# Performance work log

Hardware: AMD Instinct MI355X
Metric: run time of the kernel (lower is better)

The kernel has to match this reference:

```python
import jax, jax.numpy as jnp
import numpy as np

N_NODES = 8      # objects per graph (fixed in source)
N_AT = 16        # anchors/targets vocab: 8 colors + 8 markers
H = 128          # n_hidden
BS = 16384


def _mlp(x, W1, b1, W2, b2):
    # layers.fully_connected default activation is relu; second layer linear.
    # dropout is identity in eval mode.
    return jax.nn.relu(x @ W1 + b1) @ W2 + b2


def _edges_and_segments(bs):
    # static edge list: all ordered pairs (i,j), i != j, per graph, offset per batch
    ii, jj = np.meshgrid(np.arange(N_NODES), np.arange(N_NODES), indexing='ij')
    m = ii != jj
    base = np.stack([ii[m], jj[m]], axis=1)                      # [56, 2]
    offs = (np.arange(bs) * N_NODES)[:, None, None]
    edges = (base[None] + offs).reshape(-1, 2).astype(np.int32)  # [bs*56, 2]
    seg_ids = np.repeat(np.arange(bs), N_NODES).astype(np.int32) # [bs*8]
    return jnp.asarray(edges), jnp.asarray(seg_ids)


def setup_inputs() -> dict:
    key = jax.random.key(0)
    ks = jax.random.split(key, 14)

    anchors = jax.random.randint(ks[0], (BS,), 0, N_AT)
    n_jumps = jax.random.randint(ks[1], (BS,), 0, N_NODES)
    positions = jax.random.uniform(ks[2], (BS, N_NODES, 2), dtype=jnp.float32)
    colors = jax.random.randint(ks[3], (BS, N_NODES), 0, 8)
    markers = jax.random.randint(ks[4], (BS, N_NODES), 8, 16)  # markers live in [8,16)

    def lin(k, fan_in, fan_out):
        return jax.random.normal(k, (fan_in, fan_out), dtype=jnp.float32) / np.sqrt(fan_in)

    d_in = 2 + 8 + 8 + N_AT + N_NODES  # pos + color_oh + marker_oh + question(16+8) = 42
    z = lambda n: jnp.zeros((n,), jnp.float32)
    return {
        'anchors': anchors, 'n_jumps': n_jumps, 'positions': positions,
        'colors': colors, 'markers': markers,
        'pre_W1': lin(ks[5], d_in, H),     'pre_b1': z(H),
        'pre_W2': lin(ks[6], H, H),        'pre_b2': z(H),
        'msg_W1': lin(ks[7], 2 * H + 1, H),'msg_b1': z(H),
        'msg_W2': lin(ks[8], H, H),        'msg_b2': z(H),
        'post_W1': lin(ks[9], 2 * H, H),   'post_b1': z(H),
        'post_W2': lin(ks[10], H, H),      'post_b2': z(H),
        'out_W1': lin(ks[11], H, H),       'out_b1': z(H),
        'out_W2': lin(ks[12], H, N_AT),    'out_b2': z(N_AT),
    }


def reference(anchors, n_jumps, positions, colors, markers,
              pre_W1, pre_b1, pre_W2, pre_b2,
              msg_W1, msg_b1, msg_W2, msg_b2,
              post_W1, post_b1, post_W2, post_b2,
              out_W1, out_b1, out_W2, out_b2):
    bs = positions.shape[0]
    edges, seg_ids = _edges_and_segments(bs)
    n_total = bs * N_NODES

    col_oh = jax.nn.one_hot(colors, 8, dtype=jnp.float32).reshape(n_total, 8)
    mrk_oh = jax.nn.one_hot(markers - 8, 8, dtype=jnp.float32).reshape(n_total, 8)
    pos = positions.reshape(n_total, 2)

    # pairwise euclidean distance per edge -> [E, 1]
    dp = pos[edges[:, 0]] - pos[edges[:, 1]]
    dist = jnp.sqrt(jnp.sum(dp * dp, axis=1, keepdims=True))

    # question broadcast to every node of its graph
    q = jnp.concatenate([jax.nn.one_hot(anchors, N_AT, dtype=jnp.float32),
                         jax.nn.one_hot(n_jumps, N_NODES, dtype=jnp.float32)], axis=1)
    q = q[seg_ids]  # [bs*8, 24]

    x0 = _mlp(jnp.concatenate([pos, col_oh, mrk_oh, q], axis=1),
              pre_W1, pre_b1, pre_W2, pre_b2)  # [bs*8, H]

    # one message-passing step: gather -> MLP -> scatter(segment_sum on source idx)
    mi = jnp.concatenate([x0[edges[:, 0]], x0[edges[:, 1]], dist], axis=1)  # [E, 257]
    msgs = _mlp(mi, msg_W1, msg_b1, msg_W2, msg_b2)                          # [E, H]
    upd = jax.ops.segment_sum(msgs, edges[:, 0], num_segments=n_total)       # [bs*8, H]

    x = _mlp(jnp.concatenate([upd, x0], axis=1), post_W1, post_b1, post_W2, post_b2)

    logits = jax.ops.segment_sum(x, seg_ids, num_segments=bs)  # [bs, H]
    logits = _mlp(logits, out_W1, out_b1, out_W2, out_b2)      # [bs, 16]
    return logits
```

## Files before the change

kernel.cpp:

```cpp
#include <hip/hip_runtime.h>

#define LROW 136

typedef __bf16 bf16x8 __attribute__((ext_vector_type(8)));
typedef float  f32x4  __attribute__((ext_vector_type(4)));

#define MFMA16(a, b, c) __builtin_amdgcn_mfma_f32_16x16x32_bf16((a), (b), (c), 0, 0, 0)

__device__ __forceinline__ unsigned short f2bf(float f) {
  unsigned u = __float_as_uint(f);
  u += 0x7fffu + ((u >> 16) & 1u);
  return (unsigned short)(u >> 16);
}
__device__ __forceinline__ float bflo(unsigned v) { return __uint_as_float(v << 16); }
__device__ __forceinline__ float bfhi(unsigned v) { return __uint_as_float(v & 0xffff0000u); }

__global__ void combine_weights(
    const float* __restrict__ pre_W2, const float* __restrict__ msg_W1,
    const float* __restrict__ msg_W2, const float* __restrict__ post_W1,
    const float* __restrict__ post_W2, const float* __restrict__ out_W1,
    const float* __restrict__ out_W2, const float* __restrict__ pre_b2,
    const float* __restrict__ msg_b1, const float* __restrict__ msg_b2,
    const float* __restrict__ post_b1, const float* __restrict__ post_b2,
    const float* __restrict__ out_b1,
    unsigned short* __restrict__ WabT, unsigned short* __restrict__ WdT,
    unsigned short* __restrict__ WcT, unsigned short* __restrict__ WoT,
    unsigned short* __restrict__ Wo2T, float* __restrict__ vecs)
{
  __shared__ float part[256];
  const int b = blockIdx.x;
  const int t = threadIdx.x;
  if (b < 320) {
    const int p  = b >> 6;
    const int kp = b & 63;
    const int k  = kp * 2 + (t >> 7);
    const int n  = t & 127;
    const float* L; const float* R; unsigned short* O;
    if (p == 0)      { L = pre_W2;  R = msg_W1;             O = WabT; }
    else if (p == 1) { L = pre_W2;  R = msg_W1 + 128*128;   O = WabT + 128*128; }
    else if (p == 2) { L = pre_W2;  R = post_W1 + 128*128;  O = WdT; }
    else if (p == 3) { L = msg_W2;  R = post_W1;            O = WcT; }
    else             { L = post_W2; R = out_W1;             O = WoT; }
    const float* Lr = L + k * 128;
    float a0 = 0.f, a1 = 0.f, a2 = 0.f, a3 = 0.f;
    #pragma unroll 8
    for (int m = 0; m < 128; m += 4) {
      a0 = fmaf(Lr[m + 0], R[(m + 0) * 128 + n], a0);
      a1 = fmaf(Lr[m + 1], R[(m + 1) * 128 + n], a1);
      a2 = fmaf(Lr[m + 2], R[(m + 2) * 128 + n], a2);
      a3 = fmaf(Lr[m + 3], R[(m + 3) * 128 + n], a3);
    }
    O[n * 128 + k] = f2bf((a0 + a1) + (a2 + a3));
  } else if (b == 320) {
    for (int idx = t; idx < 16 * 128; idx += 256) {
      int o = idx >> 7, k = idx & 127;
      Wo2T[o * 128 + k] = f2bf(out_W2[k * 16 + o]);
    }
    if (t < 128) vecs[t] = msg_W1[256 * 128 + t];
  } else {
    const int n = t & 127;
    const int h = t >> 7;
    float s = 0.f;
    if (b == 321) {
      #pragma unroll 8
      for (int m = h * 64; m < h * 64 + 64; ++m)
        s = fmaf(pre_b2[m], msg_W1[m * 128 + n] + msg_W1[(128 + m) * 128 + n], s);
    } else if (b == 322) {
      #pragma unroll 8
      for (int m = h * 64; m < h * 64 + 64; ++m) {
        s = fmaf(7.f * msg_b2[m], post_W1[m * 128 + n], s);
        s = fmaf(pre_b2[m], post_W1[(128 + m) * 128 + n], s);
      }
    } else {
      #pragma unroll 8
      for (int m = h * 64; m < h * 64 + 64; ++m)
        s = fmaf(8.f * post_b2[m], out_W1[m * 128 + n], s);
    }
    part[t] = s;
    __syncthreads();
    if (t < 128) {
      float r = part[t] + part[t + 128];
      if (b == 321)      vecs[128 + t] = r + msg_b1[t];
      else if (b == 322) vecs[256 + t] = r + post_b1[t];
      else               vecs[384 + t] = r + out_b1[t];
    }
  }
}

__global__ void __launch_bounds__(256, 3) rrn_main(
    const int* __restrict__ anchors, const int* __restrict__ n_jumps,
    const float* __restrict__ positions, const int* __restrict__ colors,
    const int* __restrict__ markers, const float* __restrict__ pre_W1,
    const float* __restrict__ pre_b1,
    const unsigned short* __restrict__ WabT, const unsigned short* __restrict__ WdT,
    const unsigned short* __restrict__ WcT, const unsigned short* __restrict__ WoT,
    const unsigned short* __restrict__ Wo2T, const float* __restrict__ vecs,
    const float* __restrict__ out_b2, float* __restrict__ out)
{
  __shared__ __align__(16) char smem[54272];
  unsigned short* Ab  = (unsigned short*)(smem);
  unsigned short* Bb  = (unsigned short*)(smem + 17408);
  float* sW1          = (float*)(smem);
  float* posL         = (float*)(smem + 22016);
  int*   cmk          = (int*)(smem + 22528);
  int*   ganj         = (int*)(smem + 22784);
  unsigned short* h1  = (unsigned short*)(smem + 34816);
  unsigned short* Sph = (unsigned short*)(smem + 34816);
  unsigned short* hob = (unsigned short*)(smem + 39168);
  float* dist         = (float*)(smem + 52224);

  const int tid  = threadIdx.x;
  const int lane = tid & 63;
  const int w    = tid >> 6;
  const int l15  = lane & 15;
  const int quad = lane >> 4;
  const int g0   = blockIdx.x * 8;
  const int n0   = blockIdx.x * 64;

  for (int i = tid; i < 43 * 128; i += 256)
    sW1[i] = (i < 42 * 128) ? pre_W1[i] : pre_b1[i - 42 * 128];
  if (tid < 128) posL[tid] = positions[n0 * 2 + tid];
  else if (tid < 192) {
    int node = tid - 128;
    cmk[node] = colors[n0 + node] | ((markers[n0 + node] - 8) << 8);
  } else if (tid < 200) {
    int g = tid - 192;
    ganj[g] = anchors[g0 + g] | (n_jumps[g0 + g] << 8);
  }
  for (int i = tid; i < 512; i += 256) {
    int g = i >> 6, ii = (i >> 3) & 7, jj = i & 7;
    const float* pa = positions + (n0 + g * 8 + ii) * 2;
    const float* pb = positions + (n0 + g * 8 + jj) * 2;
    float dx = pa[0] - pb[0], dy = pa[1] - pb[1];
    dist[i] = sqrtf(dx * dx + dy * dy);
  }
  __syncthreads();

  {
    const int n  = tid & 127;
    const int rh = tid >> 7;
    for (int rr = 0; rr < 32; ++rr) {
      int r = rh * 32 + rr;
      float px = posL[r * 2], py = posL[r * 2 + 1];
      int cm = cmk[r], gn = ganj[r >> 3];
      int c = cm & 255, mk = cm >> 8;
      int a = gn & 255, nj = gn >> 8;
      float acc = sW1[42 * 128 + n]
                + px * sW1[n] + py * sW1[128 + n]
                + sW1[(2 + c) * 128 + n] + sW1[(10 + mk) * 128 + n]
                + sW1[(18 + a) * 128 + n] + sW1[(34 + nj) * 128 + n];
      h1[r * LROW + n] = f2bf(fmaxf(acc, 0.f));
    }
  }
  __syncthreads();

  f32x4 accAB[4][4];
  f32x4 accD[4][2];
  {
    f32x4 zero = {0.f, 0.f, 0.f, 0.f};
    #pragma unroll
    for (int mt = 0; mt < 4; ++mt) {
      #pragma unroll
      for (int nt = 0; nt < 4; ++nt) accAB[mt][nt] = zero;
      accD[mt][0] = zero; accD[mt][1] = zero;
    }
  }
  #pragma unroll
  for (int kb = 0; kb < 128; kb += 32) {
    const int ko = kb + quad * 8;
    bf16x8 fa[4], fb[4], fd[2];
    #pragma unroll
    for (int mt = 0; mt < 4; ++mt)
      fa[mt] = *(const bf16x8*)&h1[(mt * 16 + l15) * LROW + ko];
    #pragma unroll
    for (int nt = 0; nt < 4; ++nt)
      fb[nt] = *(const bf16x8*)&WabT[(w * 64 + nt * 16 + l15) * 128 + ko];
    #pragma unroll
    for (int dt = 0; dt < 2; ++dt)
      fd[dt] = *(const bf16x8*)&WdT[(w * 32 + dt * 16 + l15) * 128 + ko];
    #pragma unroll
    for (int mt = 0; mt < 4; ++mt) {
      #pragma unroll
      for (int nt = 0; nt < 4; ++nt)
        accAB[mt][nt] = MFMA16(fa[mt], fb[nt], accAB[mt][nt]);
      accD[mt][0] = MFMA16(fa[mt], fd[0], accD[mt][0]);
      accD[mt][1] = MFMA16(fa[mt], fd[1], accD[mt][1]);
    }
  }
  {
    unsigned short* dstbuf = (w < 2) ? Ab : Bb;
    const int cb = (w & 1) * 64;
    #pragma unroll
    for (int mt = 0; mt < 4; ++mt)
      #pragma unroll
      for (int nt = 0; nt < 4; ++nt) {
        int col = cb + nt * 16 + l15;
        #pragma unroll
        for (int r = 0; r < 4; ++r)
          dstbuf[(mt * 16 + quad * 4 + r) * LROW + col] = f2bf(accAB[mt][nt][r]);
      }
  }
  __syncthreads();

  {
    const int g   = tid >> 5;
    const int nb4 = (tid & 31) * 4;
    const float4 w1d4 = *(const float4*)&vecs[nb4];
    const float4 cab4 = *(const float4*)&vecs[128 + nb4];
    float B0[8], B1[8], B2[8], B3[8];
    #pragma unroll
    for (int j = 0; j < 8; ++j) {
      uint2 vb = *(const uint2*)&Bb[(g * 8 + j) * LROW + nb4];
      B0[j] = bflo(vb.x); B1[j] = bfhi(vb.x);
      B2[j] = bflo(vb.y); B3[j] = bfhi(vb.y);
    }
    #pragma unroll
    for (int i = 0; i < 8; ++i) {
      uint2 va = *(const uint2*)&Ab[(g * 8 + i) * LROW + nb4];
      float a0 = bflo(va.x) + cab4.x, a1 = bfhi(va.x) + cab4.y;
      float a2 = bflo(va.y) + cab4.z, a3 = bfhi(va.y) + cab4.w;
      float s0 = 0.f, s1 = 0.f, s2 = 0.f, s3 = 0.f;
      #pragma unroll
      for (int j = 0; j < 8; ++j) {
        if (j == i) continue;
        float d = dist[g * 64 + i * 8 + j];
        s0 += fmaxf(fmaf(d, w1d4.x, B0[j]) + a0, 0.f);
        s1 += fmaxf(fmaf(d, w1d4.y, B1[j]) + a1, 0.f);
        s2 += fmaxf(fmaf(d, w1d4.z, B2[j]) + a2, 0.f);
        s3 += fmaxf(fmaf(d, w1d4.w, B3[j]) + a3, 0.f);
      }
      uint2 o;
      o.x = (unsigned)f2bf(s0) | ((unsigned)f2bf(s1) << 16);
      o.y = (unsigned)f2bf(s2) | ((unsigned)f2bf(s3) << 16);
      *(uint2*)&Ab[(g * 8 + i) * LROW + nb4] = o;
    }
  }
  __syncthreads();

  {
    const unsigned short* Sb = Ab;
    #pragma unroll
    for (int kb = 0; kb < 128; kb += 32) {
      const int ko = kb + quad * 8;
      bf16x8 fa[4], fc[2];
      #pragma unroll
      for (int mt = 0; mt < 4; ++mt)
        fa[mt] = *(const bf16x8*)&Sb[(mt * 16 + l15) * LROW + ko];
      #pragma unroll
      for (int dt = 0; dt < 2; ++dt)
        fc[dt] = *(const bf16x8*)&WcT[(w * 32 + dt * 16 + l15) * 128 + ko];
      #pragma unroll
      for (int mt = 0; mt < 4; ++mt) {
        accD[mt][0] = MFMA16(fa[mt], fc[0], accD[mt][0]);
        accD[mt][1] = MFMA16(fa[mt], fc[1], accD[mt][1]);
      }
    }
    #pragma unroll
    for (int mt = 0; mt < 4; ++mt)
      #pragma unroll
      for (int dt = 0; dt < 2; ++dt) {
        int col = w * 32 + dt * 16 + l15;
        float cp = vecs[256 + col];
        f32x4 a = accD[mt][dt];
        float s = fmaxf(a[0] + cp, 0.f) + fmaxf(a[1] + cp, 0.f)
                + fmaxf(a[2] + cp, 0.f) + fmaxf(a[3] + cp, 0.f);
        s += __shfl_xor(s, 16);
        int grow = mt * 2 + (lane >= 32 ? 1 : 0);
        if ((lane & 31) < 16) Sph[grow * LROW + col] = f2bf(s);
        else                  Sph[(8 + grow) * LROW + col] = 0;
      }
  }
  __syncthreads();

  {
    f32x4 acco[2];
    f32x4 zero = {0.f, 0.f, 0.f, 0.f};
    acco[0] = zero; acco[1] = zero;
    #pragma unroll
    for (int kb = 0; kb < 128; kb += 32) {
      const int ko = kb + quad * 8;
      bf16x8 fa = *(const bf16x8*)&Sph[l15 * LROW + ko];
      #pragma unroll
      for (int dt = 0; dt < 2; ++dt) {
        bf16x8 fbv = *(const bf16x8*)&WoT[(w * 32 + dt * 16 + l15) * 128 + ko];
        acco[dt] = MFMA16(fa, fbv, acco[dt]);
      }
    }
    #pragma unroll
    for (int dt = 0; dt < 2; ++dt) {
      int col = w * 32 + dt * 16 + l15;
      float co = vecs[384 + col];
      #pragma unroll
      for (int r = 0; r < 4; ++r)
        hob[(quad * 4 + r) * LROW + col] = f2bf(fmaxf(acco[dt][r] + co, 0.f));
    }
  }
  __syncthreads();

  if (w == 0) {
    f32x4 accf = {0.f, 0.f, 0.f, 0.f};
    #pragma unroll
    for (int kb = 0; kb < 128; kb += 32) {
      const int ko = kb + quad * 8;
      bf16x8 fa  = *(const bf16x8*)&hob[l15 * LROW + ko];
      bf16x8 fbv = *(const bf16x8*)&Wo2T[l15 * 128 + ko];
      accf = MFMA16(fa, fbv, accf);
    }
    if (quad < 2) {
      float b2 = out_b2[l15];
      #pragma unroll
      for (int r = 0; r < 4; ++r) {
        int row = quad * 4 + r;
        out[(g0 + row) * 16 + l15] = accf[r] + b2;
      }
    }
  }
}

extern "C" void kernel_launch(void* const* d_in, const int* in_sizes, int n_in,
                              void* d_out, int out_size, void* d_ws, size_t ws_size,
                              hipStream_t stream) {
  const int*   anchors   = (const int*)d_in[0];
  const int*   n_jumps   = (const int*)d_in[1];
  const float* positions = (const float*)d_in[2];
  const int*   colors    = (const int*)d_in[3];
  const int*   markers   = (const int*)d_in[4];
  const float* pre_W1  = (const float*)d_in[5];
  const float* pre_b1  = (const float*)d_in[6];
  const float* pre_W2  = (const float*)d_in[7];
  const float* pre_b2  = (const float*)d_in[8];
  const float* msg_W1  = (const float*)d_in[9];
  const float* msg_b1  = (const float*)d_in[10];
  const float* msg_W2  = (const float*)d_in[11];
  const float* msg_b2  = (const float*)d_in[12];
  const float* post_W1 = (const float*)d_in[13];
  const float* post_b1 = (const float*)d_in[14];
  const float* post_W2 = (const float*)d_in[15];
  const float* post_b2 = (const float*)d_in[16];
  const float* out_W1  = (const float*)d_in[17];
  const float* out_b1  = (const float*)d_in[18];
  const float* out_W2  = (const float*)d_in[19];
  const float* out_b2  = (const float*)d_in[20];

  char* ws = (char*)d_ws;
  unsigned short* WabT = (unsigned short*)(ws);
  unsigned short* WdT  = (unsigned short*)(ws + 65536);
  unsigned short* WcT  = (unsigned short*)(ws + 98304);
  unsigned short* WoT  = (unsigned short*)(ws + 131072);
  unsigned short* Wo2T = (unsigned short*)(ws + 163840);
  float*          vecs = (float*)(ws + 167936);

  const int BS = in_sizes[0];

  combine_weights<<<324, 256, 0, stream>>>(
      pre_W2, msg_W1, msg_W2, post_W1, post_W2, out_W1, out_W2,
      pre_b2, msg_b1, msg_b2, post_b1, post_b2, out_b1,
      WabT, WdT, WcT, WoT, Wo2T, vecs);

  rrn_main<<<BS / 8, 256, 0, stream>>>(
      anchors, n_jumps, positions, colors, markers, pre_W1, pre_b1,
      WabT, WdT, WcT, WoT, Wo2T, vecs, out_b2, (float*)d_out);
}
```

Before: 177.7 us.

## Shrink shared memory and split first GEMM to fit four blocks per CU

Cuts LDS from about 54KB to 38KB by precomputing a per-graph question row (bias plus anchor and jump rows of pre_W1), so only 18 rows of pre_W1 are staged. Buffers are overlapped more aggressively and the vecs constants are cached in shared memory. The A/B and D projections are split into two MFMA passes with staged writeback and an extra barrier, which lowers live accumulator registers so launch bounds can rise to 4 blocks per CU. Float-to-bf16 conversion now uses the native __bf16 cast instead of manual rounding. The risk is more barriers and serialised MFMA phases.

```diff
diff --git a/kernel.cpp b/kernel.cpp
--- a/kernel.cpp
+++ b/kernel.cpp
@@ -2,18 +2,20 @@
 
 #define LROW 136
 
-typedef __bf16 bf16x8 __attribute__((ext_vector_type(8)));
-typedef float  f32x4  __attribute__((ext_vector_type(4)));
+typedef __bf16 bf16x8  __attribute__((ext_vector_type(8)));
+typedef __bf16 bf16x4v __attribute__((ext_vector_type(4)));
+typedef float  f32x4   __attribute__((ext_vector_type(4)));
 
 #define MFMA16(a, b, c) __builtin_amdgcn_mfma_f32_16x16x32_bf16((a), (b), (c), 0, 0, 0)
 
-__device__ __forceinline__ unsigned short f2bf(float f) {
+__device__ __forceinline__ float bflo(unsigned v) { return __uint_as_float(v << 16); }
+__device__ __forceinline__ float bfhi(unsigned v) { return __uint_as_float(v & 0xffff0000u); }
+
+__device__ __forceinline__ unsigned short f2bf_u16(float f) {
   unsigned u = __float_as_uint(f);
   u += 0x7fffu + ((u >> 16) & 1u);
   return (unsigned short)(u >> 16);
 }
-__device__ __forceinline__ float bflo(unsigned v) { return __uint_as_float(v << 16); }
-__device__ __forceinline__ float bfhi(unsigned v) { return __uint_as_float(v & 0xffff0000u); }
 
 __global__ void combine_weights(
     const float* __restrict__ pre_W2, const float* __restrict__ msg_W1,
@@ -50,11 +52,11 @@
       a2 = fmaf(Lr[m + 2], R[(m + 2) * 128 + n], a2);
       a3 = fmaf(Lr[m + 3], R[(m + 3) * 128 + n], a3);
     }
-    O[n * 128 + k] = f2bf((a0 + a1) + (a2 + a3));
+    O[n * 128 + k] = f2bf_u16((a0 + a1) + (a2 + a3));
   } else if (b == 320) {
     for (int idx = t; idx < 16 * 128; idx += 256) {
       int o = idx >> 7, k = idx & 127;
-      Wo2T[o * 128 + k] = f2bf(out_W2[k * 16 + o]);
+      Wo2T[o * 128 + k] = f2bf_u16(out_W2[k * 16 + o]);
     }
     if (t < 128) vecs[t] = msg_W1[256 * 128 + t];
   } else {
@@ -87,45 +89,51 @@
   }
 }
 
-__global__ void __launch_bounds__(256, 3) rrn_main(
+__global__ void __launch_bounds__(256, 4) rrn_main(
     const int* __restrict__ anchors, const int* __restrict__ n_jumps,
     const float* __restrict__ positions, const int* __restrict__ colors,
     const int* __restrict__ markers, const float* __restrict__ pre_W1,
     const float* __restrict__ pre_b1,
-    const unsigned short* __restrict__ WabT, const unsigned short* __restrict__ WdT,
-    const unsigned short* __restrict__ WcT, const unsigned short* __restrict__ WoT,
-    const unsigned short* __restrict__ Wo2T, const float* __restrict__ vecs,
+    const __bf16* __restrict__ WabT, const __bf16* __restrict__ WdT,
+    const __bf16* __restrict__ WcT, const __bf16* __restrict__ WoT,
+    const __bf16* __restrict__ Wo2T, const float* __restrict__ vecs,
     const float* __restrict__ out_b2, float* __restrict__ out)
 {
-  __shared__ __align__(16) char smem[54272];
-  unsigned short* Ab  = (unsigned short*)(smem);
-  unsigned short* Bb  = (unsigned short*)(smem + 17408);
-  float* sW1          = (float*)(smem);
-  float* posL         = (float*)(smem + 22016);
-  int*   cmk          = (int*)(smem + 22528);
-  int*   ganj         = (int*)(smem + 22784);
-  unsigned short* h1  = (unsigned short*)(smem + 34816);
-  unsigned short* Sph = (unsigned short*)(smem + 34816);
-  unsigned short* hob = (unsigned short*)(smem + 39168);
-  float* dist         = (float*)(smem + 52224);
+  __shared__ __align__(16) char smem[38912];
+  __bf16* Ab   = (__bf16*)(smem);
+  float*  sW1s = (float*)(smem);
+  float*  qrow = (float*)(smem + 9216);
+  float*  posL = (float*)(smem + 13312);
+  int*    cmk  = (int*)(smem + 13824);
+  __bf16* h1   = (__bf16*)(smem + 17408);
+  __bf16* Bb   = (__bf16*)(smem + 17408);
+  __bf16* Sph  = (__bf16*)(smem + 17408);
+  __bf16* hob  = (__bf16*)(smem + 21760);
+  float*  dist = (float*)(smem + 34816);
+  float*  vec  = (float*)(smem + 36864);
 
   const int tid  = threadIdx.x;
   const int lane = tid & 63;
   const int w    = tid >> 6;
   const int l15  = lane & 15;
   const int quad = lane >> 4;
+  const int colw = w * 32;
   const int g0   = blockIdx.x * 8;
   const int n0   = blockIdx.x * 64;
 
-  for (int i = tid; i < 43 * 128; i += 256)
-    sW1[i] = (i < 42 * 128) ? pre_W1[i] : pre_b1[i - 42 * 128];
+  for (int i = tid; i < 18 * 128; i += 256) sW1s[i] = pre_W1[i];
+  {
+    const int n = tid & 127;
+    for (int g = (tid >> 7); g < 8; g += 2) {
+      int a = anchors[g0 + g], nj = n_jumps[g0 + g];
+      qrow[g * 128 + n] = pre_b1[n] + pre_W1[(18 + a) * 128 + n]
+                        + pre_W1[(34 + nj) * 128 + n];
+    }
+  }
   if (tid < 128) posL[tid] = positions[n0 * 2 + tid];
   else if (tid < 192) {
     int node = tid - 128;
     cmk[node] = colors[n0 + node] | ((markers[n0 + node] - 8) << 8);
-  } else if (tid < 200) {
-    int g = tid - 192;
-    ganj[g] = anchors[g0 + g] | (n_jumps[g0 + g] << 8);
   }
   for (int i = tid; i < 512; i += 256) {
     int g = i >> 6, ii = (i >> 3) & 7, jj = i & 7;
@@ -134,6 +142,7 @@
     float dx = pa[0] - pb[0], dy = pa[1] - pb[1];
     dist[i] = sqrtf(dx * dx + dy * dy);
   }
+  for (int i = tid; i < 512; i += 256) vec[i] = vecs[i];
   __syncthreads();
 
   {
@@ -142,71 +151,89 @@
     for (int rr = 0; rr < 32; ++rr) {
       int r = rh * 32 + rr;
       float px = posL[r * 2], py = posL[r * 2 + 1];
-      int cm = cmk[r], gn = ganj[r >> 3];
+      int cm = cmk[r];
       int c = cm & 255, mk = cm >> 8;
-      int a = gn & 255, nj = gn >> 8;
-      float acc = sW1[42 * 128 + n]
-                + px * sW1[n] + py * sW1[128 + n]
-                + sW1[(2 + c) * 128 + n] + sW1[(10 + mk) * 128 + n]
-                + sW1[(18 + a) * 128 + n] + sW1[(34 + nj) * 128 + n];
-      h1[r * LROW + n] = f2bf(fmaxf(acc, 0.f));
-    }
-  }
-  __syncthreads();
-
-  f32x4 accAB[4][4];
-  f32x4 accD[4][2];
+      float acc = qrow[(r >> 3) * 128 + n]
+                + px * sW1s[n] + py * sW1s[128 + n]
+                + sW1s[(2 + c) * 128 + n] + sW1s[(10 + mk) * 128 + n];
+      h1[r * LROW + n] = (__bf16)fmaxf(acc, 0.f);
+    }
+  }
+  __syncthreads();
+
+  f32x4 acc1[4][4];
   {
     f32x4 zero = {0.f, 0.f, 0.f, 0.f};
     #pragma unroll
-    for (int mt = 0; mt < 4; ++mt) {
-      #pragma unroll
-      for (int nt = 0; nt < 4; ++nt) accAB[mt][nt] = zero;
-      accD[mt][0] = zero; accD[mt][1] = zero;
-    }
+    for (int mt = 0; mt < 4; ++mt)
+      #pragma unroll
+      for (int nt = 0; nt < 4; ++nt) acc1[mt][nt] = zero;
   }
   #pragma unroll
   for (int kb = 0; kb < 128; kb += 32) {
     const int ko = kb + quad * 8;
-    bf16x8 fa[4], fb[4], fd[2];
+    bf16x8 fa[4], fb[4];
     #pragma unroll
     for (int mt = 0; mt < 4; ++mt)
       fa[mt] = *(const bf16x8*)&h1[(mt * 16 + l15) * LROW + ko];
-    #pragma unroll
-    for (int nt = 0; nt < 4; ++nt)
-      fb[nt] = *(const bf16x8*)&WabT[(w * 64 + nt * 16 + l15) * 128 + ko];
-    #pragma unroll
-    for (int dt = 0; dt < 2; ++dt)
-      fd[dt] = *(const bf16x8*)&WdT[(w * 32 + dt * 16 + l15) * 128 + ko];
+    fb[0] = *(const bf16x8*)&WabT[(colw + l15) * 128 + ko];
+    fb[1] = *(const bf16x8*)&WabT[(colw + 16 + l15) * 128 + ko];
+    fb[2] = *(const bf16x8*)&WabT[(128 + colw + l15) * 128 + ko];
+    fb[3] = *(const bf16x8*)&WabT[(128 + colw + 16 + l15) * 128 + ko];
+    #pragma unroll
+    for (int mt = 0; mt < 4; ++mt)
+      #pragma unroll
+      for (int nt = 0; nt < 4; ++nt)
+        acc1[mt][nt] = MFMA16(fa[mt], fb[nt], acc1[mt][nt]);
+  }
+  #pragma unroll
+  for (int mt = 0; mt < 4; ++mt)
+    #pragma unroll
+    for (int nt = 0; nt < 2; ++nt) {
+      int col = colw + nt * 16 + l15;
+      #pragma unroll
+      for (int r = 0; r < 4; ++r)
+        Ab[(mt * 16 + quad * 4 + r) * LROW + col] = (__bf16)acc1[mt][nt][r];
+    }
+
+  f32x4 accD[4][2];
+  {
+    f32x4 zero = {0.f, 0.f, 0.f, 0.f};
+    #pragma unroll
+    for (int mt = 0; mt < 4; ++mt) { accD[mt][0] = zero; accD[mt][1] = zero; }
+  }
+  #pragma unroll
+  for (int kb = 0; kb < 128; kb += 32) {
+    const int ko = kb + quad * 8;
+    bf16x8 fa[4], fd[2];
+    #pragma unroll
+    for (int mt = 0; mt < 4; ++mt)
+      fa[mt] = *(const bf16x8*)&h1[(mt * 16 + l15) * LROW + ko];
+    fd[0] = *(const bf16x8*)&WdT[(colw + l15) * 128 + ko];
+    fd[1] = *(const bf16x8*)&WdT[(colw + 16 + l15) * 128 + ko];
     #pragma unroll
     for (int mt = 0; mt < 4; ++mt) {
-      #pragma unroll
-      for (int nt = 0; nt < 4; ++nt)
-        accAB[mt][nt] = MFMA16(fa[mt], fb[nt], accAB[mt][nt]);
       accD[mt][0] = MFMA16(fa[mt], fd[0], accD[mt][0]);
       accD[mt][1] = MFMA16(fa[mt], fd[1], accD[mt][1]);
     }
   }
-  {
-    unsigned short* dstbuf = (w < 2) ? Ab : Bb;
-    const int cb = (w & 1) * 64;
-    #pragma unroll
-    for (int mt = 0; mt < 4; ++mt)
-      #pragma unroll
-      for (int nt = 0; nt < 4; ++nt) {
-        int col = cb + nt * 16 + l15;
-        #pragma unroll
-        for (int r = 0; r < 4; ++r)
-          dstbuf[(mt * 16 + quad * 4 + r) * LROW + col] = f2bf(accAB[mt][nt][r]);
-      }
-  }
+  __syncthreads();
+  #pragma unroll
+  for (int mt = 0; mt < 4; ++mt)
+    #pragma unroll
+    for (int nt = 2; nt < 4; ++nt) {
+      int col = colw + (nt - 2) * 16 + l15;
+      #pragma unroll
+      for (int r = 0; r < 4; ++r)
+        Bb[(mt * 16 + quad * 4 + r) * LROW + col] = (__bf16)acc1[mt][nt][r];
+    }
   __syncthreads();
 
   {
     const int g   = tid >> 5;
     const int nb4 = (tid & 31) * 4;
-    const float4 w1d4 = *(const float4*)&vecs[nb4];
-    const float4 cab4 = *(const float4*)&vecs[128 + nb4];
+    const float4 w1d4 = *(const float4*)&vec[nb4];
+    const float4 cab4 = *(const float4*)&vec[128 + nb4];
     float B0[8], B1[8], B2[8], B3[8];
     #pragma unroll
     for (int j = 0; j < 8; ++j) {
@@ -229,16 +256,14 @@
         s2 += fmaxf(fmaf(d, w1d4.z, B2[j]) + a2, 0.f);
         s3 += fmaxf(fmaf(d, w1d4.w, B3[j]) + a3, 0.f);
       }
-      uint2 o;
-      o.x = (unsigned)f2bf(s0) | ((unsigned)f2bf(s1) << 16);
-      o.y = (unsigned)f2bf(s2) | ((unsigned)f2bf(s3) << 16);
-      *(uint2*)&Ab[(g * 8 + i) * LROW + nb4] = o;
-    }
-  }
-  __syncthreads();
-
-  {
-    const unsigned short* Sb = Ab;
+      bf16x4v o = { (__bf16)s0, (__bf16)s1, (__bf16)s2, (__bf16)s3 };
+      *(bf16x4v*)&Ab[(g * 8 + i) * LROW + nb4] = o;
+    }
+  }
+  __syncthreads();
+
+  {
+    const __bf16* Sb = Ab;
     #pragma unroll
     for (int kb = 0; kb < 128; kb += 32) {
       const int ko = kb + quad * 8;
@@ -246,9 +271,8 @@
       #pragma unroll
       for (int mt = 0; mt < 4; ++mt)
         fa[mt] = *(const bf16x8*)&Sb[(mt * 16 + l15) * LROW + ko];
-      #pragma unroll
-      for (int dt = 0; dt < 2; ++dt)
-        fc[dt] = *(const bf16x8*)&WcT[(w * 32 + dt * 16 + l15) * 128 + ko];
+      fc[0] = *(const bf16x8*)&WcT[(colw + l15) * 128 + ko];
+      fc[1] = *(const bf16x8*)&WcT[(colw + 16 + l15) * 128 + ko];
       #pragma unroll
       for (int mt = 0; mt < 4; ++mt) {
         accD[mt][0] = MFMA16(fa[mt], fc[0], accD[mt][0]);
@@ -259,15 +283,15 @@
     for (int mt = 0; mt < 4; ++mt)
       #pragma unroll
       for (int dt = 0; dt < 2; ++dt) {
-        int col = w * 32 + dt * 16 + l15;
-        float cp = vecs[256 + col];
+        int col = colw + dt * 16 + l15;
+        float cp = vec[256 + col];
         f32x4 a = accD[mt][dt];
         float s = fmaxf(a[0] + cp, 0.f) + fmaxf(a[1] + cp, 0.f)
                 + fmaxf(a[2] + cp, 0.f) + fmaxf(a[3] + cp, 0.f);
         s += __shfl_xor(s, 16);
         int grow = mt * 2 + (lane >= 32 ? 1 : 0);
-        if ((lane & 31) < 16) Sph[grow * LROW + col] = f2bf(s);
-        else                  Sph[(8 + grow) * LROW + col] = 0;
+        if ((lane & 31) < 16) Sph[grow * LROW + col] = (__bf16)s;
+        else                  Sph[(8 + grow) * LROW + col] = (__bf16)0.f;
       }
   }
   __syncthreads();
@@ -280,19 +304,18 @@
     for (int kb = 0; kb < 128; kb += 32) {
       const int ko = kb + quad * 8;
       bf16x8 fa = *(const bf16x8*)&Sph[l15 * LROW + ko];
-      #pragma unroll
-      for (int dt = 0; dt < 2; ++dt) {
-        bf16x8 fbv = *(const bf16x8*)&WoT[(w * 32 + dt * 16 + l15) * 128 + ko];
-        acco[dt] = MFMA16(fa, fbv, acco[dt]);
-      }
+      bf16x8 fb0 = *(const bf16x8*)&WoT[(colw + l15) * 128 + ko];
+      bf16x8 fb1 = *(const bf16x8*)&WoT[(colw + 16 + l15) * 128 + ko];
+      acco[0] = MFMA16(fa, fb0, acco[0]);
+      acco[1] = MFMA16(fa, fb1, acco[1]);
     }
     #pragma unroll
     for (int dt = 0; dt < 2; ++dt) {
-      int col = w * 32 + dt * 16 + l15;
-      float co = vecs[384 + col];
+      int col = colw + dt * 16 + l15;
+      float co = vec[384 + col];
       #pragma unroll
       for (int r = 0; r < 4; ++r)
-        hob[(quad * 4 + r) * LROW + col] = f2bf(fmaxf(acco[dt][r] + co, 0.f));
+        hob[(quad * 4 + r) * LROW + col] = (__bf16)fmaxf(acco[dt][r] + co, 0.f);
     }
   }
   __syncthreads();
@@ -359,5 +382,6 @@
 
   rrn_main<<<BS / 8, 256, 0, stream>>>(
       anchors, n_jumps, positions, colors, markers, pre_W1, pre_b1,
-      WabT, WdT, WcT, WoT, Wo2T, vecs, out_b2, (float*)d_out);
+      (const __bf16*)WabT, (const __bf16*)WdT, (const __bf16*)WcT,
+      (const __bf16*)WoT, (const __bf16*)Wo2T, vecs, out_b2, (float*)d_out);
 }
```

After: 155.8 us. 1.14x faster.
